# Kernel optimization log

Measured on AMD Instinct MI355X. Metric: run time of the kernel, lower is better.

## Reference

```python
import jax, jax.numpy as jnp
import numpy as np

NUM_HEADS = 32
HEAD_DIM = 128
ROPE_THETA = 10000.0


def _rope_tables(seq_len, head_dim, theta):
    inv_freq = 1.0 / (theta ** (jnp.arange(0, head_dim, 2, dtype=jnp.float32) / head_dim))
    pos = jnp.arange(seq_len, dtype=jnp.float32)
    freqs = pos[:, None] * inv_freq[None, :]            # [S, hd/2]
    emb = jnp.concatenate([freqs, freqs], axis=-1)      # [S, hd]
    return jnp.cos(emb), jnp.sin(emb)


def _rotate_half(x):
    x1, x2 = jnp.split(x, 2, axis=-1)
    return jnp.concatenate([-x2, x1], axis=-1)


def _apply_rope(x, cos, sin):
    # x: [B, S, H, D]; cos/sin: [S, D] -> unsqueeze_dim=2 broadcasting
    c = cos[None, :, None, :]
    s = sin[None, :, None, :]
    return x * c + _rotate_half(x) * s


def setup_inputs() -> dict:
    key = jax.random.key(0)
    ks = jax.random.split(key, 6)
    hidden = 4096
    B, S = 2, 4096  # global sequence = world_size * local_seq (4 * 1024)
    hidden_states = jax.random.normal(ks[0], (B, S, hidden), dtype=jnp.float32)
    # original uses torch.rand (uniform); scaled by 0.02 for numerical sanity
    q_proj = jax.random.uniform(ks[1], (hidden, hidden), dtype=jnp.float32) * 0.02
    k_proj = jax.random.uniform(ks[2], (hidden, hidden), dtype=jnp.float32) * 0.02
    v_proj = jax.random.uniform(ks[3], (hidden, hidden), dtype=jnp.float32) * 0.02
    o_proj = jax.random.uniform(ks[4], (hidden, hidden), dtype=jnp.float32) * 0.02
    return {"hidden_states": hidden_states, "q_proj": q_proj, "k_proj": k_proj,
            "v_proj": v_proj, "o_proj": o_proj, "world_size": 4}


def _ring_attention(hidden_states, q_proj, k_proj, v_proj, o_proj, world_size):
    B, S, H = hidden_states.shape
    s_local = S // world_size
    nh, hd = NUM_HEADS, HEAD_DIM
    scale = 1.0 / np.sqrt(hd).astype(np.float32)

    # rank 0 holds the first sequence shard as its local hidden states
    hs_local = hidden_states[:, :s_local]
    q = (hs_local @ q_proj.T).reshape(B, s_local, nh, hd)
    k = (hidden_states @ k_proj.T).reshape(B, S, nh, hd)
    v = (hidden_states @ v_proj.T).reshape(B, S, nh, hd)

    cos, sin = _rope_tables(S, hd, ROPE_THETA)
    q = _apply_rope(q, cos[:s_local], sin[:s_local])   # rank0 positions 0..s_local-1
    k = _apply_rope(k, cos, sin)                       # global positions per shard

    # split into per-rank KV blocks; rank 0 receives blocks W-1, W-2, ..., 0
    k_blocks = k.reshape(B, world_size, s_local, nh, hd).transpose(1, 0, 2, 3, 4)[::-1]
    v_blocks = v.reshape(B, world_size, s_local, nh, hd).transpose(1, 0, 2, 3, 4)[::-1]

    def step(carry, kv):
        attn, max_lse, denom, lse_full = carry
        k_blk, v_blk = kv
        # memory_efficient_attention_partial: non-causal partial attention + lse
        s = jnp.einsum('bqhd,bkhd->bhqk', q, k_blk) * scale
        m = jnp.max(s, axis=-1)                          # [B,H,q]
        p = jnp.exp(s - m[..., None])
        l = jnp.sum(p, axis=-1)
        lse = (m + jnp.log(l)).transpose(0, 2, 1)        # [B,q,H]
        out = jnp.einsum('bhqk,bkhd->bqhd', p / l[..., None], v_blk)
        # online-softmax merge across ring steps
        new_max = jnp.maximum(max_lse, lse)
        old_adj = jnp.exp(max_lse - new_max)[..., None]
        new_adj = jnp.exp(lse - new_max)[..., None]
        denom = old_adj * denom + new_adj
        attn = old_adj * attn + new_adj * out
        lse_full = new_max + jnp.log(jnp.exp(lse_full - new_max) + jnp.exp(lse - new_max))
        return (attn, new_max, denom, lse_full), None

    init = (jnp.zeros((B, s_local, nh, hd), jnp.float32),
            jnp.full((B, s_local, nh), -jnp.inf, jnp.float32),
            jnp.zeros((B, s_local, nh, 1), jnp.float32),
            jnp.full((B, s_local, nh), -jnp.inf, jnp.float32))
    (attn, _, denom, _), _ = jax.lax.scan(step, init, (k_blocks, v_blocks))

    attn = attn / denom
    attn = attn.astype(jnp.float16).astype(jnp.float32)  # .half() in source
    attn = attn.reshape(B, s_local, nh * hd)
    return attn @ o_proj.T


def reference(hidden_states, q_proj, k_proj, v_proj, o_proj, world_size):
    return _ring_attention(hidden_states, q_proj, k_proj, v_proj, o_proj, world_size)
```

## Files before the change

kernel.cpp:

```cpp
#include <hip/hip_runtime.h>
#include <hip/hip_bf16.h>


using bf16x8 = __attribute__((ext_vector_type(8))) short;
using f32x4  = __attribute__((ext_vector_type(4))) float;

__device__ inline unsigned short f32_to_bf16_bits(float f) {
  unsigned int u = __float_as_uint(f);
  u += 0x7FFFu + ((u >> 16) & 1u);
  return (unsigned short)(u >> 16);
}
__device__ inline float bf16_bits_to_f32(unsigned short h) {
  return __uint_as_float(((unsigned int)h) << 16);
}
__device__ inline unsigned short f32_to_bf16_fast(float f) {
  __hip_bfloat16 hb = __float2bfloat16(f);
  unsigned short us;
  __builtin_memcpy(&us, &hb, 2);
  return us;
}

__device__ __forceinline__ void load_lds16(const unsigned short* g, unsigned short* l) {
  __builtin_amdgcn_global_load_lds(
      (const __attribute__((address_space(1))) void*)g,
      (__attribute__((address_space(3))) void*)l, 16, 0, 0);
}

__global__ void cast_f32_bf16_batched(const float* __restrict__ hs,
                                      const float* __restrict__ w0,
                                      const float* __restrict__ w1,
                                      const float* __restrict__ w2,
                                      const float* __restrict__ w3,
                                      unsigned short* __restrict__ out) {
  const long hs4 = 2L * 4096 * 4096 / 4;
  const long w4  = 4096L * 4096 / 4;
  long i = (long)blockIdx.x * blockDim.x + threadIdx.x;
  long stride = (long)gridDim.x * blockDim.x;
  const long total = hs4 + 4 * w4;
  for (; i < total; i += stride) {
    const float* src;
    long j = i;
    if (j < hs4) { src = hs; }
    else {
      j -= hs4;
      long wi = j / w4;
      j -= wi * w4;
      src = (wi == 0) ? w0 : (wi == 1) ? w1 : (wi == 2) ? w2 : w3;
    }
    float4 v = reinterpret_cast<const float4*>(src)[j];
    ushort4 o;
    o.x = f32_to_bf16_bits(v.x);
    o.y = f32_to_bf16_bits(v.y);
    o.z = f32_to_bf16_bits(v.z);
    o.w = f32_to_bf16_bits(v.w);
    reinterpret_cast<ushort4*>(out)[i] = o;
  }
}

__global__ void rope_tables(float* __restrict__ cos_t, float* __restrict__ sin_t) {
  int idx = blockIdx.x * 256 + threadIdx.x;
  if (idx >= 4096 * 64) return;
  int p = idx >> 6, i = idx & 63;
  float inv = __expf(-(float)i * (9.210340371976184f / 64.0f));
  float f = (float)p * inv;
  cos_t[idx] = cosf(f);
  sin_t[idx] = sinf(f);
}

__device__ inline void storeC(float* p, float v) { *p = v; }
__device__ inline void storeC(unsigned short* p, float v) { *p = f32_to_bf16_bits(v); }

#define STG2(Gb, Lb, h, kc)                                                    \
  load_lds16((Gb) + (long)((h) * 128 + srow) * 4096 + sslot * 8 + (kc),        \
             (Lb) + tid * 8);                                                  \
  load_lds16((Gb) + (long)((h) * 128 + 64 + srow) * 4096 + sslot * 8 + (kc),   \
             (Lb) + 4096 + tid * 8);

#define MFMAQ(MH, NH)                                                          \
  _Pragma("unroll") for (int mi = 0; mi < 4; ++mi)                             \
    _Pragma("unroll") for (int ni = 0; ni < 2; ++ni)                           \
      _Pragma("unroll") for (int kk = 0; kk < 2; ++kk)                         \
        acc[(MH) * 4 + mi][(NH) * 2 + ni] =                                    \
            __builtin_amdgcn_mfma_f32_16x16x32_bf16(                           \
                a[mi][kk], b[(NH) * 2 + ni][kk],                               \
                acc[(MH) * 4 + mi][(NH) * 2 + ni], 0, 0, 0);

#define TILE(P, KC, MODE)                                                      \
  {                                                                            \
    const unsigned short* Ar = lds + wm * 16384 + (P) * 8192;                  \
    const unsigned short* Br = brw + (P) * 8192;                               \
    _Pragma("unroll") for (int mf = 0; mf < 4; ++mf) {                         \
      a[mf][0] = *reinterpret_cast<const bf16x8*>(Ar + mf * 1024 + ao0);       \
      a[mf][1] = *reinterpret_cast<const bf16x8*>(Ar + mf * 1024 + ao1);       \
    }                                                                          \
    _Pragma("unroll") for (int nf = 0; nf < 2; ++nf) {                         \
      b[nf][0] = *reinterpret_cast<const bf16x8*>(Br + boff[nf] + ao0);        \
      b[nf][1] = *reinterpret_cast<const bf16x8*>(Br + boff[nf] + ao1);        \
    }                                                                          \
    __builtin_amdgcn_s_setprio(1);                                             \
    MFMAQ(0, 0);                                                               \
    __builtin_amdgcn_s_setprio(0);                                             \
    _Pragma("unroll") for (int nf = 2; nf < 4; ++nf) {                         \
      b[nf][0] = *reinterpret_cast<const bf16x8*>(Br + boff[nf] + ao0);        \
      b[nf][1] = *reinterpret_cast<const bf16x8*>(Br + boff[nf] + ao1);        \
    }                                                                          \
    __builtin_amdgcn_s_setprio(1);                                             \
    MFMAQ(0, 1);                                                               \
    __builtin_amdgcn_s_setprio(0);                                             \
    asm volatile("s_waitcnt lgkmcnt(0)" ::: "memory");                         \
    asm volatile("s_barrier" ::: "memory");            \
    if ((MODE) == 0) {                                                         \
      STG2(Bg, lds + 32768 + (P) * 8192, 0, KC);                               \
      STG2(Bg, lds + 49152 + (P) * 8192, 1, KC);                               \
    }                                                                          \
    _Pragma("unroll") for (int mf = 0; mf < 4; ++mf) {                         \
      a[mf][0] = *reinterpret_cast<const bf16x8*>(Ar + (4 + mf) * 1024 + ao0); \
      a[mf][1] = *reinterpret_cast<const bf16x8*>(Ar + (4 + mf) * 1024 + ao1); \
    }                                                                          \
    __builtin_amdgcn_s_setprio(1);                                             \
    MFMAQ(1, 0);                                                               \
    __builtin_amdgcn_s_setprio(0);                                             \
    asm volatile("s_waitcnt lgkmcnt(0)" ::: "memory");                         \
    asm volatile("s_barrier" ::: "memory");            \
    if ((MODE) == 0) {                                                         \
      STG2(Ag, lds + (P) * 8192, 0, KC);                                       \
      STG2(Ag, lds + 16384 + (P) * 8192, 1, KC);                               \
    }                                                                          \
    __builtin_amdgcn_s_setprio(1);                                             \
    MFMAQ(1, 1);                                                               \
    __builtin_amdgcn_s_setprio(0);                                             \
    if ((MODE) == 0) asm volatile("s_waitcnt vmcnt(8)" ::: "memory");          \
    if ((MODE) == 1) asm volatile("s_waitcnt vmcnt(0)" ::: "memory");          \
    asm volatile("s_barrier" ::: "memory");       \
  }

__global__ __launch_bounds__(512, 2) void gemm_qkv(
    const unsigned short* __restrict__ hsb, const unsigned short* __restrict__ wvb,
    const unsigned short* __restrict__ wqb, const unsigned short* __restrict__ wkb,
    unsigned short* __restrict__ vTb, unsigned short* __restrict__ qob,
    unsigned short* __restrict__ kob, const float* __restrict__ cos_t,
    const float* __restrict__ sin_t, float qgain) {
  __shared__ unsigned short lds[65536];
  const int tid = threadIdx.x;
  const int id = blockIdx.x;

  const unsigned short *Ag, *Bg;
  unsigned short* Cb;
  int N, posbase;
  float gain;
  bool rope;
  if (id < 512) {
    int bn = id & 31, bm = id >> 5;
    rope = false; N = 8192; gain = 1.0f; posbase = 0;
    Ag = wvb + (long)bm * 256 * 4096;
    Bg = hsb + (long)bn * 256 * 4096;
    Cb = vTb + (long)bm * 256 * 8192 + bn * 256;
  } else if (id < 640) {
    int j = id - 512;
    int bn = j & 15, bm = (j >> 4) & 3, bz = j >> 6;
    rope = true; N = 4096; gain = qgain; posbase = bm * 256;
    Ag = hsb + (long)bz * 4096 * 4096 + (long)bm * 256 * 4096;
    Bg = wqb + (long)bn * 256 * 4096;
    Cb = qob + (long)bz * 1024 * 4096 + (long)bm * 256 * 4096 + bn * 256;
  } else {
    int j = id - 640;
    int bn = j & 15, bm = (j >> 4) & 15, bz = j >> 8;
    rope = true; N = 4096; gain = 1.0f; posbase = bm * 256;
    Ag = hsb + (long)bz * 4096 * 4096 + (long)bm * 256 * 4096;
    Bg = wkb + (long)bn * 256 * 4096;
    Cb = kob + (long)bz * 4096 * 4096 + (long)bm * 256 * 4096 + bn * 256;
  }

  const int w = tid >> 6, lane = tid & 63;
  const int wm = w >> 2, wn = w & 3;
  const int fr = lane & 15, fg = lane >> 4;
  const int ao0 = fr * 64 + ((fg ^ (fr & 7)) * 8);
  const int ao1 = fr * 64 + (((4 + fg) ^ (fr & 7)) * 8);
  const int srow = tid >> 3;
  const int sslot = (tid & 7) ^ (srow & 7);

  const unsigned short* brw =
      lds + 32768 + (wn >> 1) * 16384 + (rope ? (wn & 1) * 2048 : (wn & 1) * 4096);
  int boff[4];
#pragma unroll
  for (int nf = 0; nf < 4; ++nf)
    boff[nf] = rope ? ((nf & 1) * 1024 + (nf >> 1) * 4096) : nf * 1024;

  f32x4 acc[8][4] = {};
  bf16x8 a[4][2], b[4][2];

  STG2(Ag, lds + 0, 0, 0);     STG2(Ag, lds + 16384, 1, 0);
  STG2(Bg, lds + 32768, 0, 0); STG2(Bg, lds + 49152, 1, 0);
  STG2(Ag, lds + 8192, 0, 64);  STG2(Ag, lds + 24576, 1, 64);
  STG2(Bg, lds + 40960, 0, 64); STG2(Bg, lds + 57344, 1, 64);
  asm volatile("s_waitcnt vmcnt(8)" ::: "memory");
  asm volatile("s_barrier" ::: "memory");

  for (int ti = 0; ti < 31; ++ti) {
    TILE(0, (2 * ti + 2) * 64, 0);
    TILE(1, (2 * ti + 3) * 64, 0);
  }
  TILE(0, 0, 1);
  TILE(1, 0, 2);

  if (rope) {
    const int head = wn >> 1, q = wn & 1;
#pragma unroll
    for (int mf = 0; mf < 8; ++mf)
#pragma unroll
      for (int nf = 0; nf < 2; ++nf)
#pragma unroll
        for (int rr = 0; rr < 4; ++rr) {
          int row = wm * 128 + mf * 16 + fg * 4 + rr;
          int pos = posbase + row;
          int d = q * 32 + nf * 16 + fr;
          float c = cos_t[pos * 64 + d];
          float s = sin_t[pos * 64 + d];
          float x1 = acc[mf][nf][rr];
          float x2 = acc[mf][nf + 2][rr];
          Cb[(long)row * N + head * 128 + d] = f32_to_bf16_bits((x1 * c - x2 * s) * gain);
          Cb[(long)row * N + head * 128 + 64 + d] =
              f32_to_bf16_bits((x2 * c + x1 * s) * gain);
        }
  } else {
#pragma unroll
    for (int mf = 0; mf < 8; ++mf)
#pragma unroll
      for (int nf = 0; nf < 4; ++nf)
#pragma unroll
        for (int rr = 0; rr < 4; ++rr) {
          int row = wm * 128 + mf * 16 + fg * 4 + rr;
          int col = wn * 64 + nf * 16 + fr;
          Cb[(long)row * N + col] = f32_to_bf16_bits(acc[mf][nf][rr]);
        }
  }
}

template <typename OUT_T>
__global__ __launch_bounds__(512, 2) void gemm256(const unsigned short* __restrict__ A,
                                                  const unsigned short* __restrict__ B,
                                                  OUT_T* __restrict__ C,
                                                  long Astride_z, long Cstride_z, int N) {
  __shared__ unsigned short lds[65536];
  const int tid = threadIdx.x;
  const int bn = blockIdx.x, bm = blockIdx.y, bz = blockIdx.z;
  const unsigned short* Ag = A + (long)bz * Astride_z + (long)bm * 256 * 4096;
  const unsigned short* Bg = B + (long)bn * 256 * 4096;

  const int w = tid >> 6, lane = tid & 63;
  const int wm = w >> 2, wn = w & 3;
  const int fr = lane & 15, fg = lane >> 4;
  const int ao0 = fr * 64 + ((fg ^ (fr & 7)) * 8);
  const int ao1 = fr * 64 + (((4 + fg) ^ (fr & 7)) * 8);
  const int srow = tid >> 3;
  const int sslot = (tid & 7) ^ (srow & 7);

  const unsigned short* brw = lds + 32768 + (wn >> 1) * 16384 + (wn & 1) * 4096;
  int boff[4];
#pragma unroll
  for (int nf = 0; nf < 4; ++nf) boff[nf] = nf * 1024;

  f32x4 acc[8][4] = {};
  bf16x8 a[4][2], b[4][2];

  STG2(Ag, lds + 0, 0, 0);     STG2(Ag, lds + 16384, 1, 0);
  STG2(Bg, lds + 32768, 0, 0); STG2(Bg, lds + 49152, 1, 0);
  STG2(Ag, lds + 8192, 0, 64);  STG2(Ag, lds + 24576, 1, 64);
  STG2(Bg, lds + 40960, 0, 64); STG2(Bg, lds + 57344, 1, 64);
  asm volatile("s_waitcnt vmcnt(8)" ::: "memory");
  asm volatile("s_barrier" ::: "memory");

  for (int ti = 0; ti < 31; ++ti) {
    TILE(0, (2 * ti + 2) * 64, 0);
    TILE(1, (2 * ti + 3) * 64, 0);
  }
  TILE(0, 0, 1);
  TILE(1, 0, 2);

  OUT_T* Cb = C + (long)bz * Cstride_z + ((long)bm * 256) * N + bn * 256;
#pragma unroll
  for (int mf = 0; mf < 8; ++mf)
#pragma unroll
    for (int nf = 0; nf < 4; ++nf)
#pragma unroll
      for (int rr = 0; rr < 4; ++rr) {
        int row = wm * 128 + mf * 16 + fg * 4 + rr;
        int col = wn * 64 + nf * 16 + fr;
        storeC(Cb + (long)row * N + col, acc[mf][nf][rr]);
      }
}

__global__ __launch_bounds__(256) void attn_fwd(const unsigned short* __restrict__ qb,
                                                const unsigned short* __restrict__ kb,
                                                const unsigned short* __restrict__ vT,
                                                unsigned short* __restrict__ ob) {
  __shared__ unsigned short Ks[2][64 * 128];
  __shared__ unsigned short Vl[2][128 * 64];
  __shared__ unsigned short Ps[4][16 * 72];

  const int id = blockIdx.x;
  const int xcd = id & 7, j = id >> 3;
  const int hb = xcd + 8 * (j >> 4);
  const int qt = j & 15;
  const int h = hb & 31, b = hb >> 5;

  const int tid = threadIdx.x, w = tid >> 6, lane = tid & 63;
  const int fr = lane & 15, fg = lane >> 4;

  const unsigned short* kbase = kb + (long)b * 4096 * 4096 + h * 128;
  const unsigned short* vbase = vT + (long)h * 128 * 8192 + (long)b * 4096;

  const unsigned short* kp[4];
  const unsigned short* vp[4];
  unsigned short* kl[4];
  unsigned short* vl[4];
#pragma unroll
  for (int i = 0; i < 4; i++) {
    int c = tid + 256 * i;
    int key = c >> 4, s0 = c & 15;
    kp[i] = kbase + (long)(62 * 64 + key) * 4096 + (s0 ^ (key & 15)) * 8;
    kl[i] = (unsigned short*)&Ks[0][c * 8];
    int f0 = c >> 3, s1 = c & 7;
    vp[i] = vbase + (long)f0 * 8192 + 62 * 64 + (s1 ^ (f0 & 7)) * 8;
    vl[i] = (unsigned short*)&Vl[0][c * 8];
  }
  const int pelem = 64 * 128;

  bf16x8 qf[4];
  {
    const unsigned short* qptr =
        qb + ((long)b * 1024 + qt * 64 + w * 16 + fr) * 4096 + h * 128 + fg * 8;
#pragma unroll
    for (int c = 0; c < 4; c++) qf[c] = *reinterpret_cast<const bf16x8*>(qptr + c * 32);
  }

  f32x4 outa[8] = {};
  float m_run[4], l_run[4];
#pragma unroll
  for (int r = 0; r < 4; r++) { m_run[r] = -1e30f; l_run[r] = 0.0f; }

#pragma unroll
  for (int i = 0; i < 4; i++) {
    int c = tid + 256 * i;
    int key = c >> 4, s0 = c & 15;
    load_lds16(kbase + (long)(63 * 64 + key) * 4096 + (s0 ^ (key & 15)) * 8,
               &Ks[0][c * 8]);
    int f0 = c >> 3, s1 = c & 7;
    load_lds16(vbase + (long)f0 * 8192 + 63 * 64 + (s1 ^ (f0 & 7)) * 8,
               &Vl[0][c * 8]);
  }
  asm volatile("s_waitcnt vmcnt(0)" ::: "memory");
  asm volatile("s_barrier" ::: "memory");

  for (int it = 0; it < 64; ++it) {
    const int cur = it & 1;
    if (it < 63) {
      const int po = (cur ^ 1) * pelem;
#pragma unroll
      for (int i = 0; i < 4; i++) {
        load_lds16(kp[i], kl[i] + po);
        kp[i] -= 64 * 4096;
        load_lds16(vp[i], vl[i] + po);
        vp[i] -= 64;
      }
    }

    f32x4 sacc[4];
    __builtin_amdgcn_s_setprio(1);
#pragma unroll
    for (int ks = 0; ks < 4; ks++) {
      f32x4 aq = {0.f, 0.f, 0.f, 0.f};
#pragma unroll
      for (int cc = 0; cc < 4; cc++) {
        bf16x8 kf = *reinterpret_cast<const bf16x8*>(
            &Ks[cur][(ks * 16 + fr) * 128 + (((cc * 4 + fg) ^ fr) & 15) * 8]);
        aq = __builtin_amdgcn_mfma_f32_16x16x32_bf16(qf[cc], kf, aq, 0, 0, 0);
      }
      sacc[ks] = aq;
    }
    __builtin_amdgcn_s_setprio(0);

    float mxl[4];
    int need = 0;
#pragma unroll
    for (int r = 0; r < 4; r++) {
      mxl[r] = fmaxf(fmaxf(sacc[0][r], sacc[1][r]), fmaxf(sacc[2][r], sacc[3][r]));
      need |= (mxl[r] > m_run[r] + 11.5f) ? 1 : 0;
    }
    if (__any(need)) {
#pragma unroll
      for (int r = 0; r < 4; r++) {
        float mx = mxl[r];
        mx = fmaxf(mx, __shfl_xor(mx, 1));
        mx = fmaxf(mx, __shfl_xor(mx, 2));
        mx = fmaxf(mx, __shfl_xor(mx, 4));
        mx = fmaxf(mx, __shfl_xor(mx, 8));
        float mnew = fmaxf(m_run[r], mx);
        float ef = exp2f(m_run[r] - mnew);
        l_run[r] *= ef;
        m_run[r] = mnew;
#pragma unroll
        for (int ds = 0; ds < 8; ds++) outa[ds][r] *= ef;
      }
    }
#pragma unroll
    for (int r = 0; r < 4; r++) {
      float sum = 0.f;
#pragma unroll
      for (int ks = 0; ks < 4; ks++) {
        float pv = exp2f(sacc[ks][r] - m_run[r]);
        Ps[w][(fg * 4 + r) * 72 + ks * 16 + fr] = f32_to_bf16_fast(pv);
        sum += pv;
      }
      l_run[r] += sum;
    }

    __builtin_amdgcn_s_setprio(1);
#pragma unroll
    for (int c2 = 0; c2 < 2; c2++) {
      bf16x8 pf = *reinterpret_cast<const bf16x8*>(&Ps[w][fr * 72 + c2 * 32 + fg * 8]);
#pragma unroll
      for (int ds = 0; ds < 8; ds++) {
        int feat = ds * 16 + fr;
        int pch = ((c2 * 4 + fg) ^ (feat & 7)) & 7;
        bf16x8 vf = *reinterpret_cast<const bf16x8*>(&Vl[cur][feat * 64 + pch * 8]);
        outa[ds] = __builtin_amdgcn_mfma_f32_16x16x32_bf16(pf, vf, outa[ds], 0, 0, 0);
      }
    }
    __builtin_amdgcn_s_setprio(0);

    if (it < 63) {
      asm volatile("s_waitcnt vmcnt(0) lgkmcnt(0)" ::: "memory");
      asm volatile("s_barrier" ::: "memory");
    }
  }

#pragma unroll
  for (int r = 0; r < 4; r++) {
    float l = l_run[r];
    l += __shfl_xor(l, 1);
    l += __shfl_xor(l, 2);
    l += __shfl_xor(l, 4);
    l += __shfl_xor(l, 8);
    float inv = 1.0f / l;
    unsigned short* op =
        ob + ((long)b * 1024 + qt * 64 + w * 16 + fg * 4 + r) * 4096 + h * 128;
#pragma unroll
    for (int ds = 0; ds < 8; ds++) op[ds * 16 + fr] = f32_to_bf16_bits(outa[ds][r] * inv);
  }
}

extern "C" void kernel_launch(void* const* d_in, const int* in_sizes, int n_in,
                              void* d_out, int out_size, void* d_ws, size_t ws_size,
                              hipStream_t stream) {
  const float* hs = (const float*)d_in[0];
  const float* wq = (const float*)d_in[1];
  const float* wk = (const float*)d_in[2];
  const float* wv = (const float*)d_in[3];
  const float* wo = (const float*)d_in[4];
  float* out = (float*)d_out;

  const long hsN = 2L * 4096 * 4096;
  const long wN  = 4096L * 4096;

  unsigned short* hs_b = (unsigned short*)d_ws;
  unsigned short* wq_b = hs_b + hsN;
  unsigned short* wk_b = wq_b + wN;
  unsigned short* wv_b = wk_b + wN;
  unsigned short* wo_b = wv_b + wN;
  unsigned short* q_b  = wo_b + wN;
  unsigned short* k_b  = q_b + 2048L * 4096;
  unsigned short* vT_b = k_b + 8192L * 4096;
  unsigned short* at_b = vT_b + 8192L * 4096;
  float* cos_t = (float*)(at_b + 2048L * 4096);
  float* sin_t = cos_t + 4096 * 64;

  cast_f32_bf16_batched<<<dim3(8192), dim3(256), 0, stream>>>(
      hs, wq, wk, wv, wo, hs_b);

  rope_tables<<<dim3(1024), dim3(256), 0, stream>>>(cos_t, sin_t);

  const float qgain = 0.08838834764831845f * 1.4426950408889634f;
  gemm_qkv<<<dim3(1152), dim3(512), 0, stream>>>(
      hs_b, wv_b, wq_b, wk_b, vT_b, q_b, k_b, cos_t, sin_t, qgain);

  attn_fwd<<<dim3(1024), dim3(256), 0, stream>>>(q_b, k_b, vT_b, at_b);

  gemm256<float><<<dim3(16, 8, 1), dim3(512), 0, stream>>>(
      at_b, wo_b, out, 0L, 0L, 4096);
}
```

Before: 983.1 us.

## Split-K the output projection GEMM and fold RoPE table generation into cast kernel

The output projection GEMM launched only 128 workgroups on a 256-CU device. It is now split along K into two halves, giving 256 workgroups that write fp32 partials into the no-longer-needed hidden-state bf16 workspace, and a separate vectorized kernel sums the partials. The RoPE cos/sin table generation is merged into the cast kernel's tail to remove one launch. The split adds roughly 64MB of extra fp32 partial writes and reads plus one more kernel launch.

```diff
diff --git a/kernel.cpp b/kernel.cpp
--- a/kernel.cpp
+++ b/kernel.cpp
@@ -31,15 +31,17 @@
                                       const float* __restrict__ w1,
                                       const float* __restrict__ w2,
                                       const float* __restrict__ w3,
-                                      unsigned short* __restrict__ out) {
+                                      unsigned short* __restrict__ out,
+                                      float* __restrict__ cos_t,
+                                      float* __restrict__ sin_t) {
   const long hs4 = 2L * 4096 * 4096 / 4;
   const long w4  = 4096L * 4096 / 4;
   long i = (long)blockIdx.x * blockDim.x + threadIdx.x;
-  long stride = (long)gridDim.x * blockDim.x;
+  const long gsz = (long)gridDim.x * blockDim.x;
   const long total = hs4 + 4 * w4;
-  for (; i < total; i += stride) {
+  for (long ii = i; ii < total; ii += gsz) {
     const float* src;
-    long j = i;
+    long j = ii;
     if (j < hs4) { src = hs; }
     else {
       j -= hs4;
@@ -53,18 +55,15 @@
     o.y = f32_to_bf16_bits(v.y);
     o.z = f32_to_bf16_bits(v.z);
     o.w = f32_to_bf16_bits(v.w);
-    reinterpret_cast<ushort4*>(out)[i] = o;
-  }
-}
-
-__global__ void rope_tables(float* __restrict__ cos_t, float* __restrict__ sin_t) {
-  int idx = blockIdx.x * 256 + threadIdx.x;
-  if (idx >= 4096 * 64) return;
-  int p = idx >> 6, i = idx & 63;
-  float inv = __expf(-(float)i * (9.210340371976184f / 64.0f));
-  float f = (float)p * inv;
-  cos_t[idx] = cosf(f);
-  sin_t[idx] = sinf(f);
+    reinterpret_cast<ushort4*>(out)[ii] = o;
+  }
+  if (i < 4096 * 64) {
+    int p = (int)(i >> 6), fi = (int)(i & 63);
+    float inv = __expf(-(float)fi * (9.210340371976184f / 64.0f));
+    float f = (float)p * inv;
+    cos_t[i] = cosf(f);
+    sin_t[i] = sinf(f);
+  }
 }
 
 __device__ inline void storeC(float* p, float v) { *p = v; }
@@ -236,16 +235,19 @@
   }
 }
 
-template <typename OUT_T>
-__global__ __launch_bounds__(512, 2) void gemm256(const unsigned short* __restrict__ A,
-                                                  const unsigned short* __restrict__ B,
-                                                  OUT_T* __restrict__ C,
-                                                  long Astride_z, long Cstride_z, int N) {
+__global__ __launch_bounds__(512, 2) void gemm_o_split(
+    const unsigned short* __restrict__ A, const unsigned short* __restrict__ B,
+    float* __restrict__ P0, float* __restrict__ P1) {
   __shared__ unsigned short lds[65536];
   const int tid = threadIdx.x;
-  const int bn = blockIdx.x, bm = blockIdx.y, bz = blockIdx.z;
-  const unsigned short* Ag = A + (long)bz * Astride_z + (long)bm * 256 * 4096;
-  const unsigned short* Bg = B + (long)bn * 256 * 4096;
+  const int id = blockIdx.x;
+  const int half = id >> 7, j = id & 127;
+  const int bn = j & 15, bm = j >> 4;
+  const int koff = half * 2048;
+
+  const unsigned short* Ag = A + (long)bm * 256 * 4096 + koff;
+  const unsigned short* Bg = B + (long)bn * 256 * 4096 + koff;
+  float* Cb = (half ? P1 : P0) + (long)bm * 256 * 4096 + bn * 256;
 
   const int w = tid >> 6, lane = tid & 63;
   const int wm = w >> 2, wn = w & 3;
@@ -270,14 +272,13 @@
   asm volatile("s_waitcnt vmcnt(8)" ::: "memory");
   asm volatile("s_barrier" ::: "memory");
 
-  for (int ti = 0; ti < 31; ++ti) {
+  for (int ti = 0; ti < 15; ++ti) {
     TILE(0, (2 * ti + 2) * 64, 0);
     TILE(1, (2 * ti + 3) * 64, 0);
   }
   TILE(0, 0, 1);
   TILE(1, 0, 2);
 
-  OUT_T* Cb = C + (long)bz * Cstride_z + ((long)bm * 256) * N + bn * 256;
 #pragma unroll
   for (int mf = 0; mf < 8; ++mf)
 #pragma unroll
@@ -286,8 +287,20 @@
       for (int rr = 0; rr < 4; ++rr) {
         int row = wm * 128 + mf * 16 + fg * 4 + rr;
         int col = wn * 64 + nf * 16 + fr;
-        storeC(Cb + (long)row * N + col, acc[mf][nf][rr]);
+        Cb[(long)row * 4096 + col] = acc[mf][nf][rr];
       }
+}
+
+__global__ void add_out(const float4* __restrict__ p0, const float4* __restrict__ p1,
+                        float4* __restrict__ out, long n4) {
+  long i = (long)blockIdx.x * blockDim.x + threadIdx.x;
+  long stride = (long)gridDim.x * blockDim.x;
+  for (; i < n4; i += stride) {
+    float4 x = p0[i], y = p1[i];
+    float4 r;
+    r.x = x.x + y.x; r.y = x.y + y.y; r.z = x.z + y.z; r.w = x.w + y.w;
+    out[i] = r;
+  }
 }
 
 __global__ __launch_bounds__(256) void attn_fwd(const unsigned short* __restrict__ qb,
@@ -474,11 +487,11 @@
   unsigned short* at_b = vT_b + 8192L * 4096;
   float* cos_t = (float*)(at_b + 2048L * 4096);
   float* sin_t = cos_t + 4096 * 64;
+  float* P0 = (float*)hs_b;
+  float* P1 = P0 + 2048L * 4096;
 
   cast_f32_bf16_batched<<<dim3(8192), dim3(256), 0, stream>>>(
-      hs, wq, wk, wv, wo, hs_b);
-
-  rope_tables<<<dim3(1024), dim3(256), 0, stream>>>(cos_t, sin_t);
+      hs, wq, wk, wv, wo, hs_b, cos_t, sin_t);
 
   const float qgain = 0.08838834764831845f * 1.4426950408889634f;
   gemm_qkv<<<dim3(1152), dim3(512), 0, stream>>>(
@@ -486,6 +499,7 @@
 
   attn_fwd<<<dim3(1024), dim3(256), 0, stream>>>(q_b, k_b, vT_b, at_b);
 
-  gemm256<float><<<dim3(16, 8, 1), dim3(512), 0, stream>>>(
-      at_b, wo_b, out, 0L, 0L, 4096);
-}
+  gemm_o_split<<<dim3(256), dim3(512), 0, stream>>>(at_b, wo_b, P0, P1);
+  add_out<<<dim3(2048), dim3(256), 0, stream>>>(
+      (const float4*)P0, (const float4*)P1, (float4*)out, 2048L * 4096 / 4);
+}
```

New measurement: 966.5 us, median of 2. Within noise of the previous version (-1.7%).
